# Kernel optimization log

Hardware: AMD Instinct MI355X
Metric: run time of the kernel (lower is better)

The kernel has to match this reference:

```python
import jax, jax.numpy as jnp
import numpy as np

B, N, H, K = 2, 4096, 256, 24
IN_DIM = 2 * H + 3  # hidden*2 + 3*num_frames


def setup_inputs() -> dict:
    key = jax.random.key(0)
    ks = jax.random.split(key, 8)
    return {
        "p": jax.random.normal(ks[0], (B, N, 3), jnp.float32),
        "R": jax.random.normal(ks[1], (B, N, 3, 3), jnp.float32),
        "h": jax.random.normal(ks[2], (B, N, H), jnp.float32),
        "W1": jax.random.normal(ks[3], (IN_DIM, H), jnp.float32) * (1.0 / np.sqrt(IN_DIM)),
        "b1": jnp.zeros((H,), jnp.float32),
        "W2": jax.random.normal(ks[4], (H, H), jnp.float32) * (1.0 / np.sqrt(H)),
        "b2": jnp.zeros((H,), jnp.float32),
        "W3": jax.random.normal(ks[5], (H, H), jnp.float32) * (1.0 / np.sqrt(H)),
        "b3": jnp.zeros((H,), jnp.float32),
    }


def _knn_idx(x, k):
    # squared euclidean distances (B,N,N); nearest-k (includes self), like knn_points
    sq = jnp.sum(x * x, axis=-1)
    d = sq[:, :, None] + sq[:, None, :] - 2.0 * jnp.einsum("bnd,bmd->bnm", x, x)
    _, idx = jax.lax.top_k(-d, k)  # (B,N,K)
    return idx


def _gather(x, idx):
    # x: (B,N,D), idx: (B,N,K) -> (B,N,K,D)
    return jax.vmap(lambda a, i: a[i])(x, idx)


def reference(p, R, h, W1, b1, W2, b2, W3, b3):
    leaky = lambda x: jax.nn.leaky_relu(x, 0.1)
    idx = _knn_idx(h, K)                     # graph_type='hidden'
    p_j = _gather(p, idx)                    # (B,N,K,3)
    diff = p_j - p[:, :, None, :]            # global offset
    p_ij = jnp.einsum("bnji,bnkj->bnki", R, diff)  # local frame: R^T (p_j - p_i)
    h_j = _gather(h, idx)                    # (B,N,K,H)
    h_i = jnp.broadcast_to(h[:, :, None, :], h_j.shape)
    feat = jnp.concatenate([p_ij, h_i, h_j], axis=-1)  # (B,N,K,515)
    x = leaky(feat @ W1 + b1)
    x = leaky(x @ W2 + b2)
    x = x @ W3 + b3                          # (B,N,K,H)
    return jnp.max(x, axis=2)                # aggr='max' -> (B,N,H)
```

## Files before the change

### kernel.cpp

```cpp
#include <hip/hip_runtime.h>
#include <stdint.h>

#define BATCH 2
#define NPTS  4096
#define HDIM  256
#define KNN   24
#define NEDGE (BATCH * NPTS * KNN)
#define CAP   128
#define TGT   48

typedef __attribute__((ext_vector_type(8))) short bf16x8;
typedef __attribute__((ext_vector_type(4))) float f32x4;
typedef __attribute__((ext_vector_type(8))) unsigned short u16x8;

__device__ __forceinline__ unsigned short f2bf(float f) {
  union { float f; unsigned int u; } x; x.f = f;
  unsigned int u = x.u;
  unsigned int r = (u + 0x7fffu + ((u >> 16) & 1u)) >> 16;
  return (unsigned short)r;
}

__device__ __forceinline__ void gl2lds16(const void* g, void* l) {
  __builtin_amdgcn_global_load_lds(
      (const __attribute__((address_space(1))) unsigned int*)g,
      (__attribute__((address_space(3))) unsigned int*)l, 16, 0, 0);
}

__global__ __launch_bounds__(256) void k_sqnorm(const float* __restrict__ h,
                                                float* __restrict__ sq,
                                                unsigned short* __restrict__ hb) {
  int t = threadIdx.x, lane = t & 63, w = t >> 6;
  int row = blockIdx.x * 4 + w;
  const float* hr = h + (size_t)row * HDIM;
  float4 v = *(const float4*)(hr + lane * 4);
  ushort4 o;
  o.x = f2bf(v.x); o.y = f2bf(v.y); o.z = f2bf(v.z); o.w = f2bf(v.w);
  *(ushort4*)(hb + (size_t)row * HDIM + lane * 4) = o;
  float s = v.x * v.x + v.y * v.y + v.z * v.z + v.w * v.w;
#pragma unroll
  for (int off = 32; off; off >>= 1) s += __shfl_down(s, off);
  if (lane == 0) sq[row] = s;
}

__global__ __launch_bounds__(256) void k_convw(const float* __restrict__ W2,
                                               const float* __restrict__ W3,
                                               unsigned short* __restrict__ w2bt,
                                               unsigned short* __restrict__ w3bt) {
  int t = blockIdx.x * 256 + threadIdx.x;
  int k = t >> 8, n = t & 255;
  w2bt[n * 256 + k] = f2bf(W2[t]);
  w3bt[n * 256 + k] = f2bf(W3[t]);
}

__global__ __launch_bounds__(256) void k_dist(const unsigned short* __restrict__ hb,
                                              const float* __restrict__ sq,
                                              unsigned short* __restrict__ D16) {
  __shared__ unsigned short At[128 * 32];
  __shared__ unsigned short Bl[128 * 32];
  int b = blockIdx.z;
  int i0 = blockIdx.y * 128, j0 = blockIdx.x * 128;
  const unsigned short* A = hb + (size_t)b * NPTS * HDIM;
  int t = threadIdx.x, lane = t & 63, w = t >> 6;
  int wm = w >> 1, wn = w & 1;
  int lr = lane & 15, lk = (lane >> 4) * 8;
  f32x4 acc[4][4];
#pragma unroll
  for (int i = 0; i < 4; ++i)
#pragma unroll
    for (int j = 0; j < 4; ++j) acc[i][j] = (f32x4){0.f, 0.f, 0.f, 0.f};

  for (int k0 = 0; k0 < HDIM; k0 += 32) {
#pragma unroll
    for (int c = 0; c < 2; ++c) {
      int o = c * 256 + t;
      int row = o >> 2, cb = (o & 3) * 16;
      gl2lds16((const char*)A + ((size_t)(i0 + row) * HDIM + k0) * 2 + cb, (char*)At + o * 16);
      gl2lds16((const char*)A + ((size_t)(j0 + row) * HDIM + k0) * 2 + cb, (char*)Bl + o * 16);
    }
    __syncthreads();
    bf16x8 af[4], bfr[4];
#pragma unroll
    for (int i = 0; i < 4; ++i) af[i] = *(const bf16x8*)&At[(wm * 64 + i * 16 + lr) * 32 + lk];
#pragma unroll
    for (int j = 0; j < 4; ++j) bfr[j] = *(const bf16x8*)&Bl[(wn * 64 + j * 16 + lr) * 32 + lk];
#pragma unroll
    for (int i = 0; i < 4; ++i)
#pragma unroll
      for (int j = 0; j < 4; ++j)
        acc[i][j] = __builtin_amdgcn_mfma_f32_16x16x32_bf16(af[i], bfr[j], acc[i][j], 0, 0, 0);
    __syncthreads();
  }
#pragma unroll
  for (int i = 0; i < 4; ++i)
#pragma unroll
    for (int j = 0; j < 4; ++j)
#pragma unroll
      for (int r = 0; r < 4; ++r) {
        int gi = i0 + wm * 64 + i * 16 + (lane >> 4) * 4 + r;
        int gj = j0 + wn * 64 + j * 16 + lr;
        union { float f; unsigned u; } x;
        x.f = sq[b * NPTS + gj] - 2.f * acc[i][j][r];
        unsigned m = x.u ^ ((unsigned)((int)x.u >> 31) | 0x80000000u);
        D16[((size_t)b * NPTS + gi) * NPTS + gj] = (unsigned short)(m >> 16);
      }
}

__global__ __launch_bounds__(256) void k_topk(const unsigned short* __restrict__ D16,
                                              const float* __restrict__ h,
                                              int* __restrict__ idxout) {
  int w = threadIdx.x >> 6, lane = threadIdx.x & 63;
  int bn = blockIdx.x * 4 + w;
  int b = bn >> 12;
  const u16x8* rowv = (const u16x8*)(D16 + (size_t)bn * NPTS);

  __shared__ int s_ci[4][CAP];
  __shared__ double s_dv[4][CAP];
  __shared__ unsigned int s_cnt[4];

  if (lane == 0) s_cnt[w] = 0;

  unsigned k[64];
#pragma unroll
  for (int c = 0; c < 8; ++c) {
    u16x8 v = rowv[c * 64 + lane];
#pragma unroll
    for (int j = 0; j < 8; ++j) k[c * 8 + j] = v[j];
  }

  unsigned lo = 0, hi = 65536;
#pragma unroll 1
  for (int it = 0; it < 16; ++it) {
    unsigned mid = (lo + hi) >> 1;
    unsigned cnt = 0;
#pragma unroll
    for (int i = 0; i < 64; ++i) cnt += (k[i] < mid) ? 1u : 0u;
#pragma unroll
    for (int off = 1; off < 64; off <<= 1) cnt += __shfl_xor(cnt, off);
    if (cnt >= TGT) hi = mid; else lo = mid;
  }
  unsigned ub = hi;

#pragma unroll
  for (int i = 0; i < 64; ++i) {
    if (k[i] < ub) {
      unsigned pos = atomicAdd(&s_cnt[w], 1u);
      if (pos < CAP) s_ci[w][pos] = (i >> 3) * 512 + lane * 8 + (i & 7);
    }
  }
  int n = (int)s_cnt[w];
  if (n > CAP) n = CAP;

  const float* hbase = h + (size_t)b * NPTS * HDIM;
  const float* hn = hbase + (size_t)(bn & 4095) * HDIM;
  float4 a = *(const float4*)(hn + lane * 4);
  for (int c = 0; c < n; ++c) {
    const float* hm = hbase + (size_t)s_ci[w][c] * HDIM;
    float4 bv = *(const float4*)(hm + lane * 4);
    double d0 = (double)a.x - (double)bv.x;
    double d1 = (double)a.y - (double)bv.y;
    double d2 = (double)a.z - (double)bv.z;
    double d3 = (double)a.w - (double)bv.w;
    double d = d0 * d0 + d1 * d1 + d2 * d2 + d3 * d3;
#pragma unroll
    for (int off = 32; off; off >>= 1) d += __shfl_down(d, off);
    if (lane == 0) s_dv[w][c] = d;
  }

  for (int c = lane; c < n; c += 64) {
    double dc = s_dv[w][c];
    int ic = s_ci[w][c];
    int rank = 0;
    for (int o = 0; o < n; ++o) {
      double dv = s_dv[w][o];
      int io = s_ci[w][o];
      if (dv < dc || (dv == dc && io < ic)) ++rank;
    }
    if (rank < KNN) idxout[(size_t)bn * KNN + rank] = ic;
  }
}

__global__ __launch_bounds__(256) void k_nodefeat(const float* __restrict__ h,
                                                  const float* __restrict__ W1,
                                                  const float* __restrict__ b1,
                                                  float* __restrict__ C) {
  int ct = blockIdx.x;
  int i0 = blockIdx.y * 128;
  int wrow = (ct < 2) ? 3 : 259;
  int t = threadIdx.x, tx = t & 15, ty = t >> 4;
  __shared__ float TA[128][17];
  __shared__ float TB[16][128];
  float acc[8][8];
#pragma unroll
  for (int i = 0; i < 8; ++i)
#pragma unroll
    for (int j = 0; j < 8; ++j) acc[i][j] = 0.f;
  int srow = t >> 1, sc = (t & 1) * 8;
  int brow = t >> 4, bc = (t & 15) * 8;

  for (int k0 = 0; k0 < HDIM; k0 += 16) {
    const float* pa = &h[(size_t)(i0 + srow) * HDIM + k0 + sc];
    float4 a0 = *(const float4*)pa, a1 = *(const float4*)(pa + 4);
    const float* pb = &W1[(size_t)(wrow + k0 + brow) * HDIM + (ct & 1) * 128 + bc];
    float4 b0 = *(const float4*)pb, b1v = *(const float4*)(pb + 4);
    __syncthreads();
    TA[srow][sc + 0] = a0.x; TA[srow][sc + 1] = a0.y; TA[srow][sc + 2] = a0.z; TA[srow][sc + 3] = a0.w;
    TA[srow][sc + 4] = a1.x; TA[srow][sc + 5] = a1.y; TA[srow][sc + 6] = a1.z; TA[srow][sc + 7] = a1.w;
    *(float4*)&TB[brow][bc] = b0;
    *(float4*)&TB[brow][bc + 4] = b1v;
    __syncthreads();
#pragma unroll
    for (int kk = 0; kk < 16; ++kk) {
      float av[8], bv[8];
#pragma unroll
      for (int i = 0; i < 8; ++i) av[i] = TA[ty + 16 * i][kk];
#pragma unroll
      for (int j = 0; j < 8; ++j) bv[j] = TB[kk][tx + 16 * j];
#pragma unroll
      for (int i = 0; i < 8; ++i)
#pragma unroll
        for (int j = 0; j < 8; ++j) acc[i][j] += av[i] * bv[j];
    }
  }
#pragma unroll
  for (int i = 0; i < 8; ++i) {
    int gi = i0 + ty + 16 * i;
#pragma unroll
    for (int j = 0; j < 8; ++j) {
      int gc = ct * 128 + tx + 16 * j;
      float vv = acc[i][j];
      if (gc < 256) vv += b1[gc];
      C[(size_t)gi * 512 + gc] = vv;
    }
  }
}

__global__ __launch_bounds__(256) void k_edge1(const float* __restrict__ p,
                                               const float* __restrict__ R,
                                               const float* __restrict__ W1,
                                               const float* __restrict__ C,
                                               const int* __restrict__ idx,
                                               unsigned short* __restrict__ x1) {
  int bn = blockIdx.x;
  int b = bn >> 12;
  int t = threadIdx.x;
  __shared__ int   s_j[KNN];
  __shared__ float s_diff[KNN][3];
  __shared__ float s_pij[KNN][3];
  if (t < KNN) s_j[t] = idx[(size_t)bn * KNN + t];
  __syncthreads();
  if (t < KNN * 3) {
    int k = t / 3, d = t % 3;
    int j = s_j[k];
    s_diff[k][d] = p[((size_t)(b << 12) + j) * 3 + d] - p[(size_t)bn * 3 + d];
  }
  __syncthreads();
  if (t < KNN * 3) {
    int k = t / 3, i = t % 3;
    const float* Rp = R + (size_t)bn * 9;
    s_pij[k][i] = Rp[i] * s_diff[k][0] + Rp[3 + i] * s_diff[k][1] + Rp[6 + i] * s_diff[k][2];
  }
  __syncthreads();
  float w0 = W1[t], w1 = W1[256 + t], w2 = W1[512 + t];
  float a = C[(size_t)bn * 512 + t];
  for (int k = 0; k < KNN; ++k) {
    int j = s_j[k];
    float vv = a + C[((size_t)(b << 12) + j) * 512 + 256 + t]
             + s_pij[k][0] * w0 + s_pij[k][1] * w1 + s_pij[k][2] * w2;
    vv = vv >= 0.f ? vv : 0.1f * vv;
    x1[((size_t)bn * KNN + k) * HDIM + t] = f2bf(vv);
  }
}

__global__ __launch_bounds__(256) void k_gemm2(const unsigned short* __restrict__ A,
                                               const unsigned short* __restrict__ Bt,
                                               const float* __restrict__ bias,
                                               unsigned short* __restrict__ Out) {
  __shared__ unsigned short At[128 * 32];
  __shared__ unsigned short Bl[128 * 32];
  int t = threadIdx.x, lane = t & 63, w = t >> 6;
  int wm = w >> 1, wn = w & 1;
  int m0 = blockIdx.x * 128, n0 = blockIdx.y * 128;
  int lr = lane & 15, lk = (lane >> 4) * 8;
  f32x4 acc[4][4];
#pragma unroll
  for (int i = 0; i < 4; ++i)
#pragma unroll
    for (int j = 0; j < 4; ++j) acc[i][j] = (f32x4){0.f, 0.f, 0.f, 0.f};

  for (int k0 = 0; k0 < 256; k0 += 32) {
#pragma unroll
    for (int c = 0; c < 2; ++c) {
      int o = c * 256 + t;
      int row = o >> 2, cb = (o & 3) * 16;
      gl2lds16((const char*)A + ((size_t)(m0 + row) * 256 + k0) * 2 + cb, (char*)At + o * 16);
      gl2lds16((const char*)Bt + ((size_t)(n0 + row) * 256 + k0) * 2 + cb, (char*)Bl + o * 16);
    }
    __syncthreads();
    bf16x8 af[4], bfr[4];
#pragma unroll
    for (int i = 0; i < 4; ++i) af[i] = *(const bf16x8*)&At[(wm * 64 + i * 16 + lr) * 32 + lk];
#pragma unroll
    for (int j = 0; j < 4; ++j) bfr[j] = *(const bf16x8*)&Bl[(wn * 64 + j * 16 + lr) * 32 + lk];
#pragma unroll
    for (int i = 0; i < 4; ++i)
#pragma unroll
      for (int j = 0; j < 4; ++j)
        acc[i][j] = __builtin_amdgcn_mfma_f32_16x16x32_bf16(af[i], bfr[j], acc[i][j], 0, 0, 0);
    __syncthreads();
  }
#pragma unroll
  for (int i = 0; i < 4; ++i)
#pragma unroll
    for (int j = 0; j < 4; ++j)
#pragma unroll
      for (int r = 0; r < 4; ++r) {
        int grow = m0 + wm * 64 + i * 16 + (lane >> 4) * 4 + r;
        int gcol = n0 + wn * 64 + j * 16 + lr;
        float vv = acc[i][j][r] + bias[gcol];
        vv = vv >= 0.f ? vv : 0.1f * vv;
        Out[(size_t)grow * 256 + gcol] = f2bf(vv);
      }
}

__global__ __launch_bounds__(256) void k_gemm3max(const unsigned short* __restrict__ A,
                                                  const unsigned short* __restrict__ Bt,
                                                  const float* __restrict__ b3,
                                                  float* __restrict__ out) {
  __shared__ float Cs[128 * 129];
  unsigned short* At = (unsigned short*)Cs;
  unsigned short* Bl = At + 128 * 32;
  int t = threadIdx.x, lane = t & 63, w = t >> 6;
  int wm = w >> 1, wn = w & 1;
  int g0 = blockIdx.x * 5;
  int m0 = blockIdx.x * 120;
  int n0 = blockIdx.y * 128;
  int lr = lane & 15, lk = (lane >> 4) * 8;
  f32x4 acc[4][4];
#pragma unroll
  for (int i = 0; i < 4; ++i)
#pragma unroll
    for (int j = 0; j < 4; ++j) acc[i][j] = (f32x4){0.f, 0.f, 0.f, 0.f};

  for (int k0 = 0; k0 < 256; k0 += 32) {
#pragma unroll
    for (int c = 0; c < 2; ++c) {
      int o = c * 256 + t;
      int row = o >> 2, cb = (o & 3) * 16;
      int ar = m0 + row;
      if (ar > NEDGE - 1) ar = NEDGE - 1;
      gl2lds16((const char*)A + ((size_t)ar * 256 + k0) * 2 + cb, (char*)At + o * 16);
      gl2lds16((const char*)Bt + ((size_t)(n0 + row) * 256 + k0) * 2 + cb, (char*)Bl + o * 16);
    }
    __syncthreads();
    bf16x8 af[4], bfr[4];
#pragma unroll
    for (int i = 0; i < 4; ++i) af[i] = *(const bf16x8*)&At[(wm * 64 + i * 16 + lr) * 32 + lk];
#pragma unroll
    for (int j = 0; j < 4; ++j) bfr[j] = *(const bf16x8*)&Bl[(wn * 64 + j * 16 + lr) * 32 + lk];
#pragma unroll
    for (int i = 0; i < 4; ++i)
#pragma unroll
      for (int j = 0; j < 4; ++j)
        acc[i][j] = __builtin_amdgcn_mfma_f32_16x16x32_bf16(af[i], bfr[j], acc[i][j], 0, 0, 0);
    __syncthreads();
  }
#pragma unroll
  for (int i = 0; i < 4; ++i)
#pragma unroll
    for (int j = 0; j < 4; ++j)
#pragma unroll
      for (int r = 0; r < 4; ++r)
        Cs[(wm * 64 + i * 16 + (lane >> 4) * 4 + r) * 129 + wn * 64 + j * 16 + lr] = acc[i][j][r];
  __syncthreads();
  for (int o = t; o < 5 * 128; o += 256) {
    int g = o >> 7, col = o & 127;
    int gg = g0 + g;
    if (gg < BATCH * NPTS) {
      float mx = -3.0e38f;
#pragma unroll
      for (int r = 0; r < KNN; ++r) mx = fmaxf(mx, Cs[(g * 24 + r) * 129 + col]);
      int gcol = n0 + col;
      out[(size_t)gg * 256 + gcol] = mx + b3[gcol];
    }
  }
}

extern "C" void kernel_launch(void* const* d_in, const int* in_sizes, int n_in,
                              void* d_out, int out_size, void* d_ws, size_t ws_size,
                              hipStream_t stream) {
  const float* p  = (const float*)d_in[0];
  const float* R  = (const float*)d_in[1];
  const float* h  = (const float*)d_in[2];
  const float* W1 = (const float*)d_in[3];
  const float* b1 = (const float*)d_in[4];
  const float* W2 = (const float*)d_in[5];
  const float* b2 = (const float*)d_in[6];
  const float* W3 = (const float*)d_in[7];
  const float* b3 = (const float*)d_in[8];
  float* out = (float*)d_out;
  char* ws = (char*)d_ws;

  float*          sq   = (float*)(ws + 0);
  int*            idx  = (int*)(ws + 32768);
  float*          C    = (float*)(ws + 819200);
  unsigned short* w2bt = (unsigned short*)(ws + 17596416);
  unsigned short* w3bt = (unsigned short*)(ws + 17727488);
  char* big = ws + 17858560;
  unsigned short* x1  = (unsigned short*)big;
  unsigned short* x2  = (unsigned short*)(big + 100663296);
  unsigned short* D16 = (unsigned short*)big;
  unsigned short* hbb = (unsigned short*)(big + 134217728);

  k_sqnorm  <<<dim3(2048),     dim3(256), 0, stream>>>(h, sq, hbb);
  k_convw   <<<dim3(256),      dim3(256), 0, stream>>>(W2, W3, w2bt, w3bt);
  k_dist    <<<dim3(32, 32, 2),dim3(256), 0, stream>>>(hbb, sq, D16);
  k_topk    <<<dim3(2048),     dim3(256), 0, stream>>>(D16, h, idx);
  k_nodefeat<<<dim3(4, 64),    dim3(256), 0, stream>>>(h, W1, b1, C);
  k_edge1   <<<dim3(8192),     dim3(256), 0, stream>>>(p, R, W1, C, idx, x1);
  k_gemm2   <<<dim3(1536, 2),  dim3(256), 0, stream>>>(x1, w2bt, b2, x2);
  k_gemm3max<<<dim3(1639, 2),  dim3(256), 0, stream>>>(x2, w3bt, b3, out);
}
```

Measured before the change: 333.9 us.

## Fuse second and third MLP GEMMs keeping intermediate activations in LDS

Merges the layer-2 GEMM and the layer-3 GEMM+max kernels into one kernel per 120-edge tile. The layer-2 output is stored as bf16 in shared memory and fed directly to the layer-3 GEMM, so the large intermediate buffer never goes through global memory and one launch is dropped. In exchange, shared memory per block grows a lot and a double accumulator set raises register pressure, which lowers occupancy. Both halves of the N dimension are now computed within one block rather than across a grid dimension.

Measured after the change: 369.7 us. 1.11x slower.

```diff
diff --git a/kernel.cpp b/kernel.cpp
--- a/kernel.cpp
+++ b/kernel.cpp
@@ -271,117 +271,126 @@
   }
 }
 
-__global__ __launch_bounds__(256) void k_gemm2(const unsigned short* __restrict__ A,
-                                               const unsigned short* __restrict__ Bt,
-                                               const float* __restrict__ bias,
-                                               unsigned short* __restrict__ Out) {
+__global__ __launch_bounds__(256) void k_mlp23(const unsigned short* __restrict__ A,
+                                               const unsigned short* __restrict__ B2t,
+                                               const unsigned short* __restrict__ B3t,
+                                               const float* __restrict__ b2,
+                                               const float* __restrict__ b3,
+                                               float* __restrict__ out) {
+  __shared__ unsigned short x2t[128 * 264];
   __shared__ unsigned short At[128 * 32];
   __shared__ unsigned short Bl[128 * 32];
-  int t = threadIdx.x, lane = t & 63, w = t >> 6;
-  int wm = w >> 1, wn = w & 1;
-  int m0 = blockIdx.x * 128, n0 = blockIdx.y * 128;
-  int lr = lane & 15, lk = (lane >> 4) * 8;
-  f32x4 acc[4][4];
-#pragma unroll
-  for (int i = 0; i < 4; ++i)
-#pragma unroll
-    for (int j = 0; j < 4; ++j) acc[i][j] = (f32x4){0.f, 0.f, 0.f, 0.f};
-
-  for (int k0 = 0; k0 < 256; k0 += 32) {
-#pragma unroll
-    for (int c = 0; c < 2; ++c) {
-      int o = c * 256 + t;
-      int row = o >> 2, cb = (o & 3) * 16;
-      gl2lds16((const char*)A + ((size_t)(m0 + row) * 256 + k0) * 2 + cb, (char*)At + o * 16);
-      gl2lds16((const char*)Bt + ((size_t)(n0 + row) * 256 + k0) * 2 + cb, (char*)Bl + o * 16);
-    }
-    __syncthreads();
-    bf16x8 af[4], bfr[4];
-#pragma unroll
-    for (int i = 0; i < 4; ++i) af[i] = *(const bf16x8*)&At[(wm * 64 + i * 16 + lr) * 32 + lk];
-#pragma unroll
-    for (int j = 0; j < 4; ++j) bfr[j] = *(const bf16x8*)&Bl[(wn * 64 + j * 16 + lr) * 32 + lk];
-#pragma unroll
-    for (int i = 0; i < 4; ++i)
-#pragma unroll
-      for (int j = 0; j < 4; ++j)
-        acc[i][j] = __builtin_amdgcn_mfma_f32_16x16x32_bf16(af[i], bfr[j], acc[i][j], 0, 0, 0);
-    __syncthreads();
-  }
-#pragma unroll
-  for (int i = 0; i < 4; ++i)
-#pragma unroll
-    for (int j = 0; j < 4; ++j)
-#pragma unroll
-      for (int r = 0; r < 4; ++r) {
-        int grow = m0 + wm * 64 + i * 16 + (lane >> 4) * 4 + r;
-        int gcol = n0 + wn * 64 + j * 16 + lr;
-        float vv = acc[i][j][r] + bias[gcol];
-        vv = vv >= 0.f ? vv : 0.1f * vv;
-        Out[(size_t)grow * 256 + gcol] = f2bf(vv);
-      }
-}
-
-__global__ __launch_bounds__(256) void k_gemm3max(const unsigned short* __restrict__ A,
-                                                  const unsigned short* __restrict__ Bt,
-                                                  const float* __restrict__ b3,
-                                                  float* __restrict__ out) {
-  __shared__ float Cs[128 * 129];
-  unsigned short* At = (unsigned short*)Cs;
-  unsigned short* Bl = At + 128 * 32;
+  float* Mx = (float*)x2t;
+
   int t = threadIdx.x, lane = t & 63, w = t >> 6;
   int wm = w >> 1, wn = w & 1;
   int g0 = blockIdx.x * 5;
   int m0 = blockIdx.x * 120;
-  int n0 = blockIdx.y * 128;
   int lr = lane & 15, lk = (lane >> 4) * 8;
-  f32x4 acc[4][4];
-#pragma unroll
-  for (int i = 0; i < 4; ++i)
-#pragma unroll
-    for (int j = 0; j < 4; ++j) acc[i][j] = (f32x4){0.f, 0.f, 0.f, 0.f};
-
-  for (int k0 = 0; k0 < 256; k0 += 32) {
-#pragma unroll
-    for (int c = 0; c < 2; ++c) {
-      int o = c * 256 + t;
-      int row = o >> 2, cb = (o & 3) * 16;
-      int ar = m0 + row;
-      if (ar > NEDGE - 1) ar = NEDGE - 1;
-      gl2lds16((const char*)A + ((size_t)ar * 256 + k0) * 2 + cb, (char*)At + o * 16);
-      gl2lds16((const char*)Bt + ((size_t)(n0 + row) * 256 + k0) * 2 + cb, (char*)Bl + o * 16);
-    }
-    __syncthreads();
-    bf16x8 af[4], bfr[4];
-#pragma unroll
-    for (int i = 0; i < 4; ++i) af[i] = *(const bf16x8*)&At[(wm * 64 + i * 16 + lr) * 32 + lk];
-#pragma unroll
-    for (int j = 0; j < 4; ++j) bfr[j] = *(const bf16x8*)&Bl[(wn * 64 + j * 16 + lr) * 32 + lk];
+  int r4 = (lane >> 4) * 4;
+
+#pragma unroll 1
+  for (int nh = 0; nh < 2; ++nh) {
+    f32x4 acc[4][4];
 #pragma unroll
     for (int i = 0; i < 4; ++i)
 #pragma unroll
+      for (int j = 0; j < 4; ++j) acc[i][j] = (f32x4){0.f, 0.f, 0.f, 0.f};
+
+    for (int k0 = 0; k0 < 256; k0 += 32) {
+#pragma unroll
+      for (int c = 0; c < 2; ++c) {
+        int o = c * 256 + t;
+        int row = o >> 2, cb = (o & 3) * 16;
+        int ar = m0 + row;
+        if (ar > NEDGE - 1) ar = NEDGE - 1;
+        gl2lds16((const char*)A + ((size_t)ar * 256 + k0) * 2 + cb, (char*)At + o * 16);
+        gl2lds16((const char*)B2t + ((size_t)(nh * 128 + row) * 256 + k0) * 2 + cb, (char*)Bl + o * 16);
+      }
+      __syncthreads();
+      bf16x8 af[4], bfr[4];
+#pragma unroll
+      for (int i = 0; i < 4; ++i) af[i] = *(const bf16x8*)&At[(wm * 64 + i * 16 + lr) * 32 + lk];
+#pragma unroll
+      for (int j = 0; j < 4; ++j) bfr[j] = *(const bf16x8*)&Bl[(wn * 64 + j * 16 + lr) * 32 + lk];
+#pragma unroll
+      for (int i = 0; i < 4; ++i)
+#pragma unroll
+        for (int j = 0; j < 4; ++j)
+          acc[i][j] = __builtin_amdgcn_mfma_f32_16x16x32_bf16(af[i], bfr[j], acc[i][j], 0, 0, 0);
+      __syncthreads();
+    }
+#pragma unroll
+    for (int i = 0; i < 4; ++i)
+#pragma unroll
       for (int j = 0; j < 4; ++j)
-        acc[i][j] = __builtin_amdgcn_mfma_f32_16x16x32_bf16(af[i], bfr[j], acc[i][j], 0, 0, 0);
-    __syncthreads();
-  }
-#pragma unroll
-  for (int i = 0; i < 4; ++i)
-#pragma unroll
-    for (int j = 0; j < 4; ++j)
-#pragma unroll
-      for (int r = 0; r < 4; ++r)
-        Cs[(wm * 64 + i * 16 + (lane >> 4) * 4 + r) * 129 + wn * 64 + j * 16 + lr] = acc[i][j][r];
-  __syncthreads();
-  for (int o = t; o < 5 * 128; o += 256) {
-    int g = o >> 7, col = o & 127;
-    int gg = g0 + g;
-    if (gg < BATCH * NPTS) {
-      float mx = -3.0e38f;
-#pragma unroll
-      for (int r = 0; r < KNN; ++r) mx = fmaxf(mx, Cs[(g * 24 + r) * 129 + col]);
-      int gcol = n0 + col;
-      out[(size_t)gg * 256 + gcol] = mx + b3[gcol];
-    }
+#pragma unroll
+        for (int r = 0; r < 4; ++r) {
+          int row = wm * 64 + i * 16 + r4 + r;
+          int col = nh * 128 + wn * 64 + j * 16 + lr;
+          float vv = acc[i][j][r] + b2[col];
+          vv = vv >= 0.f ? vv : 0.1f * vv;
+          x2t[row * 264 + col] = f2bf(vv);
+        }
+    __syncthreads();
+  }
+
+  f32x4 acc2[2][4][4];
+#pragma unroll
+  for (int nh = 0; nh < 2; ++nh) {
+#pragma unroll
+    for (int i = 0; i < 4; ++i)
+#pragma unroll
+      for (int j = 0; j < 4; ++j) acc2[nh][i][j] = (f32x4){0.f, 0.f, 0.f, 0.f};
+
+#pragma unroll 1
+    for (int k0 = 0; k0 < 256; k0 += 32) {
+#pragma unroll
+      for (int c = 0; c < 2; ++c) {
+        int o = c * 256 + t;
+        int row = o >> 2, cb = (o & 3) * 16;
+        gl2lds16((const char*)B3t + ((size_t)(nh * 128 + row) * 256 + k0) * 2 + cb, (char*)Bl + o * 16);
+      }
+      __syncthreads();
+      bf16x8 af[4], bfr[4];
+#pragma unroll
+      for (int i = 0; i < 4; ++i) af[i] = *(const bf16x8*)&x2t[(wm * 64 + i * 16 + lr) * 264 + k0 + lk];
+#pragma unroll
+      for (int j = 0; j < 4; ++j) bfr[j] = *(const bf16x8*)&Bl[(wn * 64 + j * 16 + lr) * 32 + lk];
+#pragma unroll
+      for (int i = 0; i < 4; ++i)
+#pragma unroll
+        for (int j = 0; j < 4; ++j)
+          acc2[nh][i][j] = __builtin_amdgcn_mfma_f32_16x16x32_bf16(af[i], bfr[j], acc2[nh][i][j], 0, 0, 0);
+      __syncthreads();
+    }
+  }
+
+#pragma unroll
+  for (int nh = 0; nh < 2; ++nh) {
+#pragma unroll
+    for (int i = 0; i < 4; ++i)
+#pragma unroll
+      for (int j = 0; j < 4; ++j)
+#pragma unroll
+        for (int r = 0; r < 4; ++r) {
+          int row = wm * 64 + i * 16 + r4 + r;
+          int col = wn * 64 + j * 16 + lr;
+          Mx[row * 129 + col] = acc2[nh][i][j][r];
+        }
+    __syncthreads();
+    for (int o = t; o < 5 * 128; o += 256) {
+      int g = o >> 7, col = o & 127;
+      int gg = g0 + g;
+      if (gg < BATCH * NPTS) {
+        float mx = -3.0e38f;
+#pragma unroll
+        for (int r = 0; r < KNN; ++r) mx = fmaxf(mx, Mx[(g * 24 + r) * 129 + col]);
+        int gcol = nh * 128 + col;
+        out[(size_t)gg * 256 + gcol] = mx + b3[gcol];
+      }
+    }
+    __syncthreads();
   }
 }
 
@@ -407,7 +416,6 @@
   unsigned short* w3bt = (unsigned short*)(ws + 17727488);
   char* big = ws + 17858560;
   unsigned short* x1  = (unsigned short*)big;
-  unsigned short* x2  = (unsigned short*)(big + 100663296);
   unsigned short* D16 = (unsigned short*)big;
   unsigned short* hbb = (unsigned short*)(big + 134217728);
 
@@ -417,6 +425,5 @@
   k_topk    <<<dim3(2048),     dim3(256), 0, stream>>>(D16, h, idx);
   k_nodefeat<<<dim3(4, 64),    dim3(256), 0, stream>>>(h, W1, b1, C);
   k_edge1   <<<dim3(8192),     dim3(256), 0, stream>>>(p, R, W1, C, idx, x1);
-  k_gemm2   <<<dim3(1536, 2),  dim3(256), 0, stream>>>(x1, w2bt, b2, x2);
-  k_gemm3max<<<dim3(1639, 2),  dim3(256), 0, stream>>>(x2, w3bt, b3, out);
-}
+  k_mlp23   <<<dim3(1639),     dim3(256), 0, stream>>>(x1, w2bt, w3bt, b2, b3, out);
+}
```
